# Performance work log

Hardware: AMD Instinct MI355X
Metric: run time of the kernel (lower is better)

The kernel has to match this reference:

```python
import jax, jax.numpy as jnp
import numpy as np

N_HEAD, D_K = 16, 64  # from init_kwargs (d_v == d_k)

def setup_inputs() -> dict:
    key = jax.random.key(0)
    ks = jax.random.split(key, 8)
    B, S, D, DFF = 8, 1024, 1024, 4096
    s = 1.0 / np.sqrt(D)
    return {
        "enc_input": jax.random.normal(ks[0], (B, S, D), jnp.float32),
        "mask": jnp.ones((B, 1, S), jnp.int32),
        "gap": 1,
        "wq": jax.random.normal(ks[1], (D, N_HEAD * D_K), jnp.float32) * s,
        "wk": jax.random.normal(ks[2], (D, N_HEAD * D_K), jnp.float32) * s,
        "wv": jax.random.normal(ks[3], (D, N_HEAD * D_K), jnp.float32) * s,
        "wo": jax.random.normal(ks[4], (N_HEAD * D_K, D), jnp.float32) * s,
        "w1": jax.random.normal(ks[5], (D, DFF), jnp.float32) * s,
        "b1": jnp.zeros((DFF,), jnp.float32),
        "w2": jax.random.normal(ks[6], (DFF, D), jnp.float32) * (1.0 / np.sqrt(DFF)),
        "b2": jnp.zeros((D,), jnp.float32),
    }

def reference(enc_input, mask, gap, wq, wk, wv, wo, w1, b1, w2, b2):
    # dropout=0, use_layer_norm=0, adapter=0 are hard-coded in EncoderLayer.__init__
    B, S, D = enc_input.shape
    H, dk = N_HEAD, D_K
    temperature = dk ** 0.5

    q = (enc_input @ wq).reshape(B, S, H, dk).transpose(0, 2, 1, 3)  # [B,H,S,dk]
    k = (enc_input @ wk).reshape(B, S, H, dk).transpose(0, 2, 1, 3)
    v = (enc_input @ wv).reshape(B, S, H, dk).transpose(0, 2, 1, 3)

    attn = jnp.einsum('bhqd,bhkd->bhqk', q / temperature, k)  # [B,H,S,S]
    # mask [B,1,S] -> unsqueeze head dim -> [B,1,1,S]
    attn = jnp.where(mask[:, None] == 0, jnp.float32(-1e9), attn)
    attn = jax.nn.softmax(attn, axis=-1)

    ctx = jnp.einsum('bhqk,bhkd->bhqd', attn, v)          # [B,H,S,dk]
    ctx = ctx.transpose(0, 2, 1, 3).reshape(B, S, H * dk)  # [B,S,D]
    enc = ctx @ wo + enc_input                              # attn residual

    ffn = jax.nn.relu(enc @ w1 + b1) @ w2 + b2
    out = ffn + enc                                         # ffn residual
    return out, attn
```

## Files before the change

kernel.cpp:

```cpp
#include <hip/hip_runtime.h>
#include <hip/hip_bf16.h>
#include <stdint.h>

typedef __bf16 bf16x8 __attribute__((ext_vector_type(8)));
typedef float  f32x4  __attribute__((ext_vector_type(4)));

typedef __attribute__((address_space(1))) void gvoid;
typedef __attribute__((address_space(3))) void lvoid;

__device__ __forceinline__ void async16(void* lds, const void* g) {
    __builtin_amdgcn_global_load_lds((gvoid*)g, (lvoid*)lds, 16, 0, 0);
}

__device__ __forceinline__ float fexp2(float x) {
    return __builtin_amdgcn_exp2f(x);
}

__global__ void prep_all(const float* __restrict__ X, __hip_bfloat16* __restrict__ Xb,
                         const float* __restrict__ wq, const float* __restrict__ wk,
                         const float* __restrict__ wv, const float* __restrict__ wo,
                         const float* __restrict__ w1, const float* __restrict__ w2,
                         __hip_bfloat16* __restrict__ Wcat,
                         __hip_bfloat16* __restrict__ Wot,
                         __hip_bfloat16* __restrict__ W1t,
                         __hip_bfloat16* __restrict__ W2t) {
    const int tix = blockIdx.x;
    if (tix >= 12288) {
        const int bi = tix - 12288;
        const int tid = threadIdx.y * 32 + threadIdx.x;
        const long i = ((long)bi * 256 + tid) * 4;
        float4 v = *(const float4*)(X + i);
        __hip_bfloat162* d = (__hip_bfloat162*)(Xb + i);
        d[0] = __float22bfloat162_rn(make_float2(v.x, v.y));
        d[1] = __float22bfloat162_rn(make_float2(v.z, v.w));
        return;
    }
    __shared__ float t[32][33];
    const float* in;
    __hip_bfloat16* out;
    int R, C, cx, cy;
    if (tix < 4096) {
        int wid = tix >> 10, tile = tix & 1023;
        const float* srcs[4] = {wq, wk, wv, wo};
        __hip_bfloat16* dsts[4] = {Wcat, Wcat + 1024 * 1024, Wcat + 2 * 1024 * 1024, Wot};
        in = srcs[wid]; out = dsts[wid];
        R = 1024; C = 1024; cx = tile & 31; cy = tile >> 5;
    } else if (tix < 8192) {
        int tile = tix - 4096;
        in = w1; out = W1t; R = 1024; C = 4096;
        cx = tile & 127; cy = tile >> 7;
    } else {
        int tile = tix - 8192;
        in = w2; out = W2t; R = 4096; C = 1024;
        cx = tile & 31; cy = tile >> 5;
    }
    const int c0 = cx * 32, r0 = cy * 32;
    const int tx = threadIdx.x, ty = threadIdx.y;
#pragma unroll
    for (int i = 0; i < 4; ++i) {
        int r = r0 + ty + i * 8;
        t[ty + i * 8][tx] = in[(long)r * C + c0 + tx];
    }
    __syncthreads();
#pragma unroll
    for (int i = 0; i < 4; ++i) {
        int c = c0 + ty + i * 8;
        out[(long)c * R + r0 + tx] = __float2bfloat16(t[tx][ty + i * 8]);
    }
}

#define RBAR asm volatile("s_barrier" ::: "memory")

__global__ void __launch_bounds__(256, 2)
attn_fused(const __hip_bfloat16* __restrict__ QKb,
           const __hip_bfloat16* __restrict__ Vt,
           const int* __restrict__ mask,
           float* __restrict__ attn,
           __hip_bfloat16* __restrict__ Ctx) {
    __shared__ __align__(16) __hip_bfloat16 sK[128 * 64];
    __shared__ __align__(16) __hip_bfloat16 sV[2][64 * 128];
    __shared__ __align__(16) __hip_bfloat16 sP[128 * 64];
    __shared__ float smadd[1024];

    const int tid = threadIdx.x, lane = tid & 63, wave = tid >> 6;
    const int r16 = lane & 15, kg = lane >> 4;
    const float SC2 = 0.125f * 1.44269504f;

    const int dd = blockIdx.x;
    const int wgt = (dd & 7) * 128 + (dd >> 3);
    const int xblk = wgt & 7, z = wgt >> 3;
    const int b = z >> 4, h = z & 15;
    const int row0 = xblk * 128;
    const int wrow = wave * 32;

    const __hip_bfloat16* Qz = QKb + ((long)b * 1024 + row0) * 2048 + h * 64;
    const __hip_bfloat16* Kz = QKb + (long)b * 1024 * 2048 + 1024 + h * 64;
    const __hip_bfloat16* Vz = Vt + (long)z * 64 * 1024;
    float* attnZ = attn + (long)z * 1024 * 1024 + (long)row0 * 1024;

    for (int i = tid; i < 1024; i += 256)
        smadd[i] = mask[b * 1024 + i] ? 0.f : -1.5e9f;

    bf16x8 qa[2][2];
#pragma unroll
    for (int m = 0; m < 2; ++m)
#pragma unroll
        for (int kf = 0; kf < 2; ++kf)
            qa[m][kf] = *(const bf16x8*)(Qz + (long)(wrow + m * 16 + r16) * 2048 + kf * 32 + kg * 8);

    float lrow[2][4];
#pragma unroll
    for (int m = 0; m < 2; ++m)
#pragma unroll
        for (int i = 0; i < 4; ++i) lrow[m][i] = 0.f;

    const int ssw = (r16 & 7) << 4;

    auto stageK = [&](char* dst, int ct) {
#pragma unroll
        for (int j = 0; j < 4; ++j) {
            int c = wave * 4 + j;
            int s = c * 8 + (lane >> 3);
            int cb = (lane & 7) * 16;
            async16(dst + c * 1024,
                    (const char*)(Kz + (long)(ct * 128 + s) * 2048) + (cb ^ ((s & 7) << 4)));
        }
    };
    auto stageV = [&](int ct, int buf) {
#pragma unroll
        for (int j = 0; j < 4; ++j) {
            int c = wave * 4 + j;
            int dv = c * 4 + (lane >> 4);
            int cb = (lane & 15) * 16;
            async16((char*)sV[buf] + c * 1024,
                    (const char*)(Vz + (long)dv * 1024 + ct * 128) + (cb ^ ((dv & 7) << 4)));
        }
    };

    char* kbuf0 = (char*)sK;
    char* kbuf1 = (char*)sP;
    stageK(kbuf0, 0);

    for (int ct = 0; ct < 8; ++ct) {
        asm volatile("s_waitcnt vmcnt(0)" ::: "memory");
        __syncthreads();
        if (ct < 7) stageK((ct & 1) ? kbuf0 : kbuf1, ct + 1);
        const char* base = (ct & 1) ? kbuf1 : kbuf0;

        f32x4 sacc[2][8];
#pragma unroll
        for (int m = 0; m < 2; ++m)
#pragma unroll
            for (int nf = 0; nf < 8; ++nf) sacc[m][nf] = f32x4{0.f, 0.f, 0.f, 0.f};

        __builtin_amdgcn_s_setprio(1);
#pragma unroll
        for (int nf = 0; nf < 8; ++nf) {
            const char* kr = base + (nf * 16 + r16) * 128;
            bf16x8 bv0 = *(const bf16x8*)(kr + ((kg * 16) ^ ssw));
            bf16x8 bv1 = *(const bf16x8*)(kr + ((64 + kg * 16) ^ ssw));
#pragma unroll
            for (int m = 0; m < 2; ++m) {
                sacc[m][nf] = __builtin_amdgcn_mfma_f32_16x16x32_bf16(qa[m][0], bv0, sacc[m][nf], 0, 0, 0);
                sacc[m][nf] = __builtin_amdgcn_mfma_f32_16x16x32_bf16(qa[m][1], bv1, sacc[m][nf], 0, 0, 0);
            }
        }
        __builtin_amdgcn_s_setprio(0);

        float madd[8];
#pragma unroll
        for (int nf = 0; nf < 8; ++nf) madd[nf] = smadd[ct * 128 + nf * 16 + r16];

#pragma unroll
        for (int m = 0; m < 2; ++m)
#pragma unroll
            for (int i = 0; i < 4; ++i) {
                float ts = 0.f;
#pragma unroll
                for (int nf = 0; nf < 8; ++nf)
                    ts += fexp2(sacc[m][nf][i] * SC2 + madd[nf]);
#pragma unroll
                for (int o = 1; o < 16; o <<= 1) ts += __shfl_xor(ts, o);
                lrow[m][i] += ts;
            }
    }

    float rinv[2][4];
#pragma unroll
    for (int m = 0; m < 2; ++m)
#pragma unroll
        for (int i = 0; i < 4; ++i) rinv[m][i] = 1.0f / lrow[m][i];

    f32x4 oacc[2][4];
#pragma unroll
    for (int m = 0; m < 2; ++m)
#pragma unroll
        for (int nf = 0; nf < 4; ++nf) oacc[m][nf] = f32x4{0.f, 0.f, 0.f, 0.f};

    __syncthreads();
    stageK((char*)sK, 0);
    stageV(0, 0);
    asm volatile("s_waitcnt vmcnt(0)" ::: "memory");
    __syncthreads();

    for (int ct = 0; ct < 8; ++ct) {
        f32x4 sacc[2][8];
#pragma unroll
        for (int m = 0; m < 2; ++m)
#pragma unroll
            for (int nf = 0; nf < 8; ++nf) sacc[m][nf] = f32x4{0.f, 0.f, 0.f, 0.f};

        __builtin_amdgcn_s_setprio(1);
#pragma unroll
        for (int nf = 0; nf < 8; ++nf) {
            const char* kr = (const char*)sK + (nf * 16 + r16) * 128;
            bf16x8 bv0 = *(const bf16x8*)(kr + ((kg * 16) ^ ssw));
            bf16x8 bv1 = *(const bf16x8*)(kr + ((64 + kg * 16) ^ ssw));
#pragma unroll
            for (int m = 0; m < 2; ++m) {
                sacc[m][nf] = __builtin_amdgcn_mfma_f32_16x16x32_bf16(qa[m][0], bv0, sacc[m][nf], 0, 0, 0);
                sacc[m][nf] = __builtin_amdgcn_mfma_f32_16x16x32_bf16(qa[m][1], bv1, sacc[m][nf], 0, 0, 0);
            }
        }
        __builtin_amdgcn_s_setprio(0);

        RBAR;
        if (ct < 7) {
            stageK((char*)sK, ct + 1);
            stageV(ct + 1, (ct + 1) & 1);
        }
        asm volatile("" ::: "memory");

        float madd[8];
#pragma unroll
        for (int nf = 0; nf < 8; ++nf) madd[nf] = smadd[ct * 128 + nf * 16 + r16];

        const char* sVb = (const char*)sV[ct & 1];

#pragma unroll
        for (int half = 0; half < 2; ++half) {
#pragma unroll
            for (int m = 0; m < 2; ++m)
#pragma unroll
                for (int nf = 0; nf < 4; ++nf) {
                    const int nfg = half * 4 + nf;
                    const int scol = nfg * 16 + r16;
                    const int scl = nf * 16 + r16;
#pragma unroll
                    for (int i = 0; i < 4; ++i) {
                        int q = wrow + m * 16 + kg * 4 + i;
                        float p = fexp2(sacc[m][nfg][i] * SC2 + madd[nfg]) * rinv[m][i];
                        __builtin_nontemporal_store(p, attnZ + (long)q * 1024 + ct * 128 + scol);
                        *(__hip_bfloat16*)((char*)sP + q * 128 + ((scl * 2) ^ ((q & 7) << 4))) =
                            __float2bfloat16(p);
                    }
                }

            __builtin_amdgcn_s_setprio(1);
#pragma unroll
            for (int ks = 0; ks < 2; ++ks) {
                const int ksg = half * 2 + ks;
                bf16x8 pa[2], vv[4];
#pragma unroll
                for (int m = 0; m < 2; ++m)
                    pa[m] = *(const bf16x8*)((const char*)sP + (wrow + m * 16 + r16) * 128 +
                                             ((ks * 64 + kg * 16) ^ ssw));
#pragma unroll
                for (int nf = 0; nf < 4; ++nf)
                    vv[nf] = *(const bf16x8*)(sVb + (nf * 16 + r16) * 256 +
                                              ((ksg * 64 + kg * 16) ^ ssw));
#pragma unroll
                for (int m = 0; m < 2; ++m)
#pragma unroll
                    for (int nf = 0; nf < 4; ++nf)
                        oacc[m][nf] = __builtin_amdgcn_mfma_f32_16x16x32_bf16(pa[m], vv[nf], oacc[m][nf], 0, 0, 0);
            }
            __builtin_amdgcn_s_setprio(0);
        }

        if (ct < 7) {
            asm volatile("s_waitcnt vmcnt(63)" ::: "memory");
            RBAR;
        }
    }

#pragma unroll
    for (int m = 0; m < 2; ++m)
#pragma unroll
        for (int nf = 0; nf < 4; ++nf)
#pragma unroll
            for (int i = 0; i < 4; ++i) {
                int q = wrow + m * 16 + kg * 4 + i;
                Ctx[((long)b * 1024 + row0 + q) * 1024 + h * 64 + nf * 16 + r16] =
                    __float2bfloat16(oacc[m][nf][i]);
            }
}

#define RDA(BUF, PM, ML, KS) \
    (*(const bf16x8*)(aRd + (BUF)*32768 + (PM)*16384 + (ML)*2048 + ((((KS)*64) + kg*16) ^ sw)))
#define RDB(BUF, PN, NL, KS) \
    (*(const bf16x8*)(bRd + (BUF)*32768 + (PN)*16384 + (NL)*2048 + ((((KS)*64) + kg*16) ^ sw)))
#define LOAD_A(BUF, PM)                          \
    _Pragma("unroll") for (int ml = 0; ml < 4; ++ml) \
    _Pragma("unroll") for (int ks = 0; ks < 2; ++ks) \
        a[ml][ks] = RDA(BUF, PM, ml, ks)
#define LOAD_B(DST, BUF, PN)                     \
    _Pragma("unroll") for (int nl = 0; nl < 2; ++nl) \
    _Pragma("unroll") for (int ks = 0; ks < 2; ++ks) \
        DST[nl][ks] = RDB(BUF, PN, nl, ks)
#define MFMA16(PM, PN, BB)                                                   \
    __builtin_amdgcn_s_setprio(1);                                           \
    _Pragma("unroll") for (int ks = 0; ks < 2; ++ks)                         \
    _Pragma("unroll") for (int ml = 0; ml < 4; ++ml)                         \
    _Pragma("unroll") for (int nl = 0; nl < 2; ++nl)                         \
        acc[(PM)*4 + ml][(PN)*2 + nl] = __builtin_amdgcn_mfma_f32_16x16x32_bf16( \
            a[ml][ks], BB[nl][ks], acc[(PM)*4 + ml][(PN)*2 + nl], 0, 0, 0);  \
    __builtin_amdgcn_s_setprio(0)
#define BAR asm volatile("s_barrier" ::: "memory")

__global__ void __launch_bounds__(512, 2)
gemm256(const __hip_bfloat16* __restrict__ A, int lda,
        const __hip_bfloat16* __restrict__ Bt, int ldb,
        int K, int Mtiles,
        const float* __restrict__ bias, int relu,
        __hip_bfloat16* __restrict__ C, int ldc) {
    __shared__ __align__(16) char lds[131072];
    const int NT = K >> 6;
    const int tid = threadIdx.x, lane = tid & 63, wave = tid >> 6;
    const int r16 = lane & 15, kg = lane >> 4;
    const int wr = wave >> 2, wc = wave & 3;
    const int sw = (r16 & 7) << 4;

    const int nwg = gridDim.x;
    const int q8 = nwg >> 3, r8 = nwg & 7;
    const int xcd = blockIdx.x & 7, rest = blockIdx.x >> 3;
    const int wg = (xcd < r8 ? xcd * (q8 + 1) : r8 * (q8 + 1) + (xcd - r8) * q8) + rest;
    const int tm = wg % Mtiles, tn = wg / Mtiles;
    const long row0 = (long)tm * 256, col0 = (long)tn * 256;

    const int idx = tid >> 3;
    const int slotp = ((tid & 7) ^ (idx & 7)) * 8;
    const __hip_bfloat16* aSrc[4];
    const __hip_bfloat16* bSrc[4];
#pragma unroll
    for (int j = 0; j < 4; ++j) {
        long ar = row0 + (j & 1) * 128 + (j >> 1) * 64 + idx;
        aSrc[j] = A + ar * lda + slotp;
        long br = col0 + ((j & 1) * 2 + (tid >> 8)) * 64 + (j >> 1) * 32 + (idx & 31);
        bSrc[j] = Bt + br * ldb + slotp;
    }

    char* ldsA = lds;
    char* ldsB = lds + 65536;
    const int stDst = wave * 1024;
    auto stA = [&](int v, int j) {
        async16(ldsA + ((v & 1) << 15) + (j << 13) + stDst, aSrc[j] + (v << 6));
    };
    auto stB = [&](int v, int j) {
        async16(ldsB + ((v & 1) << 15) + (j << 13) + stDst, bSrc[j] + (v << 6));
    };

    stA(0, 0); stA(0, 1); stB(0, 0); stB(0, 1);
    stA(0, 2); stA(0, 3); stB(0, 2); stB(0, 3);
    stA(1, 0); stA(1, 1); stB(1, 0); stB(1, 1);
    asm volatile("s_waitcnt vmcnt(4)" ::: "memory");
    BAR;

    f32x4 acc[8][4] = {};
    const char* aRd = ldsA + wr * 8192 + r16 * 128;
    const char* bRd = ldsB + wc * 4096 + r16 * 128;

    for (int u = 0; u < NT; u += 2) {
        const bool more = (u + 2) < NT;
        bf16x8 a[4][2], b0[2][2], b1[2][2];

        LOAD_A(0, 0);
        LOAD_B(b0, 0, 0);
        stA(u + 1, 2); stA(u + 1, 3);
        MFMA16(0, 0, b0);
        BAR;

        LOAD_B(b1, 0, 1);
        stB(u + 1, 2); stB(u + 1, 3);
        MFMA16(0, 1, b1);
        BAR;

        LOAD_A(0, 1);
        if (more) { stA(u + 2, 0); stA(u + 2, 1); }
        MFMA16(1, 0, b0);
        BAR;

        if (more) {
            stB(u + 2, 0); stB(u + 2, 1);
            asm volatile("s_waitcnt vmcnt(4)" ::: "memory");
        } else {
            asm volatile("s_waitcnt vmcnt(0)" ::: "memory");
        }
        MFMA16(1, 1, b1);
        BAR;

        LOAD_A(1, 0);
        LOAD_B(b0, 1, 0);
        if (more) { stA(u + 2, 2); stA(u + 2, 3); }
        MFMA16(0, 0, b0);
        BAR;

        LOAD_B(b1, 1, 1);
        if (more) { stB(u + 2, 2); stB(u + 2, 3); }
        MFMA16(0, 1, b1);
        BAR;

        LOAD_A(1, 1);
        if (more) { stA(u + 3, 0); stA(u + 3, 1); }
        MFMA16(1, 0, b0);
        BAR;

        if (more) {
            stB(u + 3, 0); stB(u + 3, 1);
            asm volatile("s_waitcnt vmcnt(4)" ::: "memory");
        }
        MFMA16(1, 1, b1);
        BAR;
    }

    const long crow = row0 + wr * 128, ccol = col0 + wc * 64;
#pragma unroll
    for (int mf = 0; mf < 8; ++mf)
#pragma unroll
        for (int nf = 0; nf < 4; ++nf) {
            const long col = ccol + nf * 16 + r16;
            const float bs = bias ? bias[col] : 0.f;
#pragma unroll
            for (int i = 0; i < 4; ++i) {
                const long row = crow + mf * 16 + kg * 4 + i;
                float v = acc[mf][nf][i] + bs;
                if (relu) v = fmaxf(v, 0.f);
                C[row * (long)ldc + col] = __float2bfloat16(v);
            }
        }
}

#define RDB128(BUF, NL, KS) \
    (*(const bf16x8*)(bRd + (BUF)*16384 + (NL)*2048 + ((((KS)*64) + kg*16) ^ sw)))
#define LOAD_B128(DST, BUF)                      \
    _Pragma("unroll") for (int nl = 0; nl < 2; ++nl) \
    _Pragma("unroll") for (int ks = 0; ks < 2; ++ks) \
        DST[nl][ks] = RDB128(BUF, nl, ks)
#define MFMA16N(PM, BB)                                                      \
    __builtin_amdgcn_s_setprio(1);                                           \
    _Pragma("unroll") for (int ks = 0; ks < 2; ++ks)                         \
    _Pragma("unroll") for (int ml = 0; ml < 4; ++ml)                         \
    _Pragma("unroll") for (int nl = 0; nl < 2; ++nl)                         \
        acc[(PM)*4 + ml][nl] = __builtin_amdgcn_mfma_f32_16x16x32_bf16(      \
            a[ml][ks], BB[nl][ks], acc[(PM)*4 + ml][nl], 0, 0, 0);           \
    __builtin_amdgcn_s_setprio(0)

__global__ void __launch_bounds__(512, 2)
gemm256n128(const __hip_bfloat16* __restrict__ A, int lda,
            const __hip_bfloat16* __restrict__ Bt, int ldb,
            int K, int Mtiles,
            const float* __restrict__ bias, int relu,
            const float* __restrict__ resf,
            const __hip_bfloat16* __restrict__ resb, int ldres,
            float* __restrict__ Cf, __hip_bfloat16* __restrict__ Cb, int ldc) {
    __shared__ __align__(16) char lds[98304];
    const int NT = K >> 6;
    const int tid = threadIdx.x, lane = tid & 63, wave = tid >> 6;
    const int r16 = lane & 15, kg = lane >> 4;
    const int wr = wave >> 2, wc = wave & 3;
    const int sw = (r16 & 7) << 4;

    const int nwg = gridDim.x;
    const int q8 = nwg >> 3, r8 = nwg & 7;
    const int xcd = blockIdx.x & 7, rest = blockIdx.x >> 3;
    const int wg = (xcd < r8 ? xcd * (q8 + 1) : r8 * (q8 + 1) + (xcd - r8) * q8) + rest;
    const int tm = wg % Mtiles, tn = wg / Mtiles;
    const long row0 = (long)tm * 256, col0 = (long)tn * 128;

    const int idx = tid >> 3;
    const int slotp = ((tid & 7) ^ (idx & 7)) * 8;
    const __hip_bfloat16* aSrc[4];
    const __hip_bfloat16* bSrc[2];
#pragma unroll
    for (int j = 0; j < 4; ++j) {
        long ar = row0 + (j & 1) * 128 + (j >> 1) * 64 + idx;
        aSrc[j] = A + ar * lda + slotp;
    }
#pragma unroll
    for (int j = 0; j < 2; ++j) {
        long br = col0 + j * 64 + idx;
        bSrc[j] = Bt + br * ldb + slotp;
    }

    char* ldsA = lds;
    char* ldsB = lds + 65536;
    const int stDst = wave * 1024;
    auto stA = [&](int v, int j) {
        async16(ldsA + ((v & 1) << 15) + (j << 13) + stDst, aSrc[j] + (v << 6));
    };
    auto stB = [&](int v, int j) {
        async16(ldsB + ((v & 1) << 14) + (j << 13) + stDst, bSrc[j] + (v << 6));
    };

    stA(0, 0); stA(0, 1); stA(0, 2); stA(0, 3);
    stB(0, 0); stB(0, 1);
    stA(1, 0); stA(1, 1);
    stB(1, 0); stB(1, 1);
    asm volatile("s_waitcnt vmcnt(4)" ::: "memory");
    BAR;

    f32x4 acc[8][2] = {};
    const char* aRd = ldsA + wr * 8192 + r16 * 128;
    const char* bRd = ldsB + wc * 4096 + r16 * 128;

    for (int u = 0; u < NT; u += 2) {
        const bool more = (u + 2) < NT;
        bf16x8 a[4][2], b0[2][2], b1[2][2];

        LOAD_A(0, 0);
        LOAD_B128(b0, 0);
        stA(u + 1, 2); stA(u + 1, 3);
        MFMA16N(0, b0);
        BAR;

        LOAD_A(0, 1);
        if (more) {
            stA(u + 2, 0); stA(u + 2, 1);
            stB(u + 2, 0); stB(u + 2, 1);
            asm volatile("s_waitcnt vmcnt(4)" ::: "memory");
        } else {
            asm volatile("s_waitcnt vmcnt(0)" ::: "memory");
        }
        MFMA16N(1, b0);
        BAR;

        LOAD_A(1, 0);
        LOAD_B128(b1, 1);
        if (more) { stA(u + 2, 2); stA(u + 2, 3); }
        MFMA16N(0, b1);
        BAR;

        LOAD_A(1, 1);
        if (more) {
            stA(u + 3, 0); stA(u + 3, 1);
            stB(u + 3, 0); stB(u + 3, 1);
            asm volatile("s_waitcnt vmcnt(4)" ::: "memory");
        }
        MFMA16N(1, b1);
        BAR;
    }

    const long crow = row0 + wr * 128, ccol = col0 + wc * 32;
#pragma unroll
    for (int mf = 0; mf < 8; ++mf)
#pragma unroll
        for (int nf = 0; nf < 2; ++nf) {
            const long col = ccol + nf * 16 + r16;
            const float bs = bias ? bias[col] : 0.f;
#pragma unroll
            for (int i = 0; i < 4; ++i) {
                const long row = crow + mf * 16 + kg * 4 + i;
                float v = acc[mf][nf][i] + bs;
                if (relu) v = fmaxf(v, 0.f);
                if (resf) v += resf[row * (long)ldres + col];
                if (resb) v += __bfloat162float(resb[row * (long)ldres + col]);
                const long off = row * (long)ldc + col;
                if (Cf) Cf[off] = v;
                if (Cb) Cb[off] = __float2bfloat16(v);
            }
        }
}

__global__ void __launch_bounds__(512, 2)
gemm_v(const __hip_bfloat16* __restrict__ A, int lda,
       const __hip_bfloat16* __restrict__ Bt, int ldb,
       int K,
       __hip_bfloat16* __restrict__ Vt) {
    __shared__ __align__(16) char lds[98304];
    const int NT = K >> 6;
    const int tid = threadIdx.x, lane = tid & 63, wave = tid >> 6;
    const int r16 = lane & 15, kg = lane >> 4;
    const int wr = wave >> 2, wc = wave & 3;
    const int sw = (r16 & 7) << 4;

    const int nwg = gridDim.x;
    const int q8 = nwg >> 3, r8 = nwg & 7;
    const int xcd = blockIdx.x & 7, rest = blockIdx.x >> 3;
    const int wg = (xcd < r8 ? xcd * (q8 + 1) : r8 * (q8 + 1) + (xcd - r8) * q8) + rest;
    const int tm = wg & 31, tn = wg >> 5;
    const long row0 = (long)tm * 256, col0 = (long)tn * 128;

    const int idx = tid >> 3;
    const int slotp = ((tid & 7) ^ (idx & 7)) * 8;
    const __hip_bfloat16* aSrc[4];
    const __hip_bfloat16* bSrc[2];
#pragma unroll
    for (int j = 0; j < 4; ++j) {
        long ar = row0 + (j & 1) * 128 + (j >> 1) * 64 + idx;
        aSrc[j] = A + ar * lda + slotp;
    }
#pragma unroll
    for (int j = 0; j < 2; ++j) {
        long br = col0 + j * 64 + idx;
        bSrc[j] = Bt + br * ldb + slotp;
    }

    char* ldsA = lds;
    char* ldsB = lds + 65536;
    const int stDst = wave * 1024;
    auto stA = [&](int v, int j) {
        async16(ldsA + ((v & 1) << 15) + (j << 13) + stDst, aSrc[j] + (v << 6));
    };
    auto stB = [&](int v, int j) {
        async16(ldsB + ((v & 1) << 14) + (j << 13) + stDst, bSrc[j] + (v << 6));
    };

    stA(0, 0); stA(0, 1); stA(0, 2); stA(0, 3);
    stB(0, 0); stB(0, 1);
    stA(1, 0); stA(1, 1);
    stB(1, 0); stB(1, 1);
    asm volatile("s_waitcnt vmcnt(4)" ::: "memory");
    BAR;

    f32x4 acc[8][2] = {};
    const char* aRd = ldsA + wr * 8192 + r16 * 128;
    const char* bRd = ldsB + wc * 4096 + r16 * 128;

    for (int u = 0; u < NT; u += 2) {
        const bool more = (u + 2) < NT;
        bf16x8 a[4][2], b0[2][2], b1[2][2];

        LOAD_A(0, 0);
        LOAD_B128(b0, 0);
        stA(u + 1, 2); stA(u + 1, 3);
        MFMA16N(0, b0);
        BAR;

        LOAD_A(0, 1);
        if (more) {
            stA(u + 2, 0); stA(u + 2, 1);
            stB(u + 2, 0); stB(u + 2, 1);
            asm volatile("s_waitcnt vmcnt(4)" ::: "memory");
        } else {
            asm volatile("s_waitcnt vmcnt(0)" ::: "memory");
        }
        MFMA16N(1, b0);
        BAR;

        LOAD_A(1, 0);
        LOAD_B128(b1, 1);
        if (more) { stA(u + 2, 2); stA(u + 2, 3); }
        MFMA16N(0, b1);
        BAR;

        LOAD_A(1, 1);
        if (more) {
            stA(u + 3, 0); stA(u + 3, 1);
            stB(u + 3, 0); stB(u + 3, 1);
            asm volatile("s_waitcnt vmcnt(4)" ::: "memory");
        }
        MFMA16N(1, b1);
        BAR;
    }

    __hip_bfloat16* sT = (__hip_bfloat16*)lds;
    {
        const int cls = wc * 32;
        const int rls = wr * 128 + kg * 4;
#pragma unroll
        for (int mf = 0; mf < 8; ++mf)
#pragma unroll
            for (int nf = 0; nf < 2; ++nf) {
                int cl = cls + nf * 16 + r16;
                int rl = rls + mf * 16;
                __hip_bfloat162 lo = __float22bfloat162_rn(make_float2(acc[mf][nf][0], acc[mf][nf][1]));
                __hip_bfloat162 hi = __float22bfloat162_rn(make_float2(acc[mf][nf][2], acc[mf][nf][3]));
                *(__hip_bfloat162*)(&sT[cl * 264 + rl]) = lo;
                *(__hip_bfloat162*)(&sT[cl * 264 + rl + 2]) = hi;
            }
    }
    __syncthreads();
    {
        const int b = (int)(row0 >> 10);
        const int s_base = (int)(row0 & 1023);
#pragma unroll
        for (int j = 0; j < 8; ++j) {
            int dl = wave * 16 + j * 2 + (lane >> 5);
            int sc = (lane & 31) * 8;
            bf16x8 v = *(const bf16x8*)(&sT[dl * 264 + sc]);
            int dg = (int)col0 + dl;
            int z = b * 16 + (dg >> 6);
            int d = dg & 63;
            *(bf16x8*)(Vt + ((long)z * 64 + d) * 1024 + s_base + sc) = v;
        }
    }
}

extern "C" void kernel_launch(void* const* d_in, const int* in_sizes, int n_in,
                              void* d_out, int out_size, void* d_ws, size_t ws_size,
                              hipStream_t stream) {
    const int B = 8, S = 1024, D = 1024, DFF = 4096;
    const long SD = (long)B * S * D;

    const float* X  = (const float*)d_in[0];
    const int*  msk = (const int*)d_in[1];
    const float* wq = (const float*)d_in[3];
    const float* wk = (const float*)d_in[4];
    const float* wv = (const float*)d_in[5];
    const float* wo = (const float*)d_in[6];
    const float* w1 = (const float*)d_in[7];
    const float* b1 = (const float*)d_in[8];
    const float* w2 = (const float*)d_in[9];
    const float* b2 = (const float*)d_in[10];

    float* out  = (float*)d_out;
    float* attn = out + SD;

    char* ws = (char*)d_ws;
    auto alloc = [&](size_t bytes) {
        char* p = ws;
        ws += (bytes + 255) & ~(size_t)255;
        return p;
    };
    __hip_bfloat16* Xb   = (__hip_bfloat16*)alloc(SD * 2);
    __hip_bfloat16* QKb  = (__hip_bfloat16*)alloc(SD * 4);
    __hip_bfloat16* Vt   = (__hip_bfloat16*)alloc(SD * 2);
    __hip_bfloat16* Ctx  = (__hip_bfloat16*)alloc(SD * 2);
    __hip_bfloat16* EncB = (__hip_bfloat16*)alloc(SD * 2);
    __hip_bfloat16* Hb   = (__hip_bfloat16*)alloc((long)B * S * DFF * 2);
    __hip_bfloat16* Wcat = (__hip_bfloat16*)alloc((long)3 * D * D * 2);
    __hip_bfloat16* Wot  = (__hip_bfloat16*)alloc((long)D * D * 2);
    __hip_bfloat16* W1t  = (__hip_bfloat16*)alloc((long)D * DFF * 2);
    __hip_bfloat16* W2t  = (__hip_bfloat16*)alloc((long)D * DFF * 2);
    (void)ws_size; (void)in_sizes; (void)n_in; (void)out_size;

    dim3 tb(32, 8);
    prep_all<<<dim3(12288 + 8192), tb, 0, stream>>>(X, Xb, wq, wk, wv, wo, w1, w2,
                                                    Wcat, Wot, W1t, W2t);

    gemm256<<<dim3(32 * 8), 512, 0, stream>>>(
        Xb, D, Wcat, D, D, 32, nullptr, 0, QKb, 2048);

    gemm_v<<<dim3(32 * 8), 512, 0, stream>>>(
        Xb, D, Wcat + (long)2048 * 1024, D, D, Vt);

    attn_fused<<<dim3(1024), 256, 0, stream>>>(QKb, Vt, msk, attn, Ctx);

    gemm256n128<<<dim3(32 * 8), 512, 0, stream>>>(
        Ctx, D, Wot, D, D, 32,
        nullptr, 0, X, nullptr, D,
        nullptr, EncB, D);

    gemm256<<<dim3(32 * 16), 512, 0, stream>>>(
        EncB, D, W1t, D, D, 32, b1, 1, Hb, DFF);

    gemm256n128<<<dim3(32 * 8), 512, 0, stream>>>(
        Hb, DFF, W2t, DFF, DFF, 32,
        b2, 0, nullptr, EncB, D,
        out, nullptr, D);
}
```

Baseline: 500.8 us.

## Merge QK and V projection GEMMs into one launch; nontemporal fp32 stores

```diff
diff --git a/kernel.cpp b/kernel.cpp
--- a/kernel.cpp
+++ b/kernel.cpp
@@ -139,6 +139,7 @@
 
     char* kbuf0 = (char*)sK;
     char* kbuf1 = (char*)sP;
+    kbuf1 = (char*)sV[0];
     stageK(kbuf0, 0);
 
     for (int ct = 0; ct < 8; ++ct) {
@@ -317,129 +318,6 @@
             a[ml][ks], BB[nl][ks], acc[(PM)*4 + ml][(PN)*2 + nl], 0, 0, 0);  \
     __builtin_amdgcn_s_setprio(0)
 #define BAR asm volatile("s_barrier" ::: "memory")
-
-__global__ void __launch_bounds__(512, 2)
-gemm256(const __hip_bfloat16* __restrict__ A, int lda,
-        const __hip_bfloat16* __restrict__ Bt, int ldb,
-        int K, int Mtiles,
-        const float* __restrict__ bias, int relu,
-        __hip_bfloat16* __restrict__ C, int ldc) {
-    __shared__ __align__(16) char lds[131072];
-    const int NT = K >> 6;
-    const int tid = threadIdx.x, lane = tid & 63, wave = tid >> 6;
-    const int r16 = lane & 15, kg = lane >> 4;
-    const int wr = wave >> 2, wc = wave & 3;
-    const int sw = (r16 & 7) << 4;
-
-    const int nwg = gridDim.x;
-    const int q8 = nwg >> 3, r8 = nwg & 7;
-    const int xcd = blockIdx.x & 7, rest = blockIdx.x >> 3;
-    const int wg = (xcd < r8 ? xcd * (q8 + 1) : r8 * (q8 + 1) + (xcd - r8) * q8) + rest;
-    const int tm = wg % Mtiles, tn = wg / Mtiles;
-    const long row0 = (long)tm * 256, col0 = (long)tn * 256;
-
-    const int idx = tid >> 3;
-    const int slotp = ((tid & 7) ^ (idx & 7)) * 8;
-    const __hip_bfloat16* aSrc[4];
-    const __hip_bfloat16* bSrc[4];
-#pragma unroll
-    for (int j = 0; j < 4; ++j) {
-        long ar = row0 + (j & 1) * 128 + (j >> 1) * 64 + idx;
-        aSrc[j] = A + ar * lda + slotp;
-        long br = col0 + ((j & 1) * 2 + (tid >> 8)) * 64 + (j >> 1) * 32 + (idx & 31);
-        bSrc[j] = Bt + br * ldb + slotp;
-    }
-
-    char* ldsA = lds;
-    char* ldsB = lds + 65536;
-    const int stDst = wave * 1024;
-    auto stA = [&](int v, int j) {
-        async16(ldsA + ((v & 1) << 15) + (j << 13) + stDst, aSrc[j] + (v << 6));
-    };
-    auto stB = [&](int v, int j) {
-        async16(ldsB + ((v & 1) << 15) + (j << 13) + stDst, bSrc[j] + (v << 6));
-    };
-
-    stA(0, 0); stA(0, 1); stB(0, 0); stB(0, 1);
-    stA(0, 2); stA(0, 3); stB(0, 2); stB(0, 3);
-    stA(1, 0); stA(1, 1); stB(1, 0); stB(1, 1);
-    asm volatile("s_waitcnt vmcnt(4)" ::: "memory");
-    BAR;
-
-    f32x4 acc[8][4] = {};
-    const char* aRd = ldsA + wr * 8192 + r16 * 128;
-    const char* bRd = ldsB + wc * 4096 + r16 * 128;
-
-    for (int u = 0; u < NT; u += 2) {
-        const bool more = (u + 2) < NT;
-        bf16x8 a[4][2], b0[2][2], b1[2][2];
-
-        LOAD_A(0, 0);
-        LOAD_B(b0, 0, 0);
-        stA(u + 1, 2); stA(u + 1, 3);
-        MFMA16(0, 0, b0);
-        BAR;
-
-        LOAD_B(b1, 0, 1);
-        stB(u + 1, 2); stB(u + 1, 3);
-        MFMA16(0, 1, b1);
-        BAR;
-
-        LOAD_A(0, 1);
-        if (more) { stA(u + 2, 0); stA(u + 2, 1); }
-        MFMA16(1, 0, b0);
-        BAR;
-
-        if (more) {
-            stB(u + 2, 0); stB(u + 2, 1);
-            asm volatile("s_waitcnt vmcnt(4)" ::: "memory");
-        } else {
-            asm volatile("s_waitcnt vmcnt(0)" ::: "memory");
-        }
-        MFMA16(1, 1, b1);
-        BAR;
-
-        LOAD_A(1, 0);
-        LOAD_B(b0, 1, 0);
-        if (more) { stA(u + 2, 2); stA(u + 2, 3); }
-        MFMA16(0, 0, b0);
-        BAR;
-
-        LOAD_B(b1, 1, 1);
-        if (more) { stB(u + 2, 2); stB(u + 2, 3); }
-        MFMA16(0, 1, b1);
-        BAR;
-
-        LOAD_A(1, 1);
-        if (more) { stA(u + 3, 0); stA(u + 3, 1); }
-        MFMA16(1, 0, b0);
-        BAR;
-
-        if (more) {
-            stB(u + 3, 0); stB(u + 3, 1);
-            asm volatile("s_waitcnt vmcnt(4)" ::: "memory");
-        }
-        MFMA16(1, 1, b1);
-        BAR;
-    }
-
-    const long crow = row0 + wr * 128, ccol = col0 + wc * 64;
-#pragma unroll
-    for (int mf = 0; mf < 8; ++mf)
-#pragma unroll
-        for (int nf = 0; nf < 4; ++nf) {
-            const long col = ccol + nf * 16 + r16;
-            const float bs = bias ? bias[col] : 0.f;
-#pragma unroll
-            for (int i = 0; i < 4; ++i) {
-                const long row = crow + mf * 16 + kg * 4 + i;
-                float v = acc[mf][nf][i] + bs;
-                if (relu) v = fmaxf(v, 0.f);
-                C[row * (long)ldc + col] = __float2bfloat16(v);
-            }
-        }
-}
-
 #define RDB128(BUF, NL, KS) \
     (*(const bf16x8*)(bRd + (BUF)*16384 + (NL)*2048 + ((((KS)*64) + kg*16) ^ sw)))
 #define LOAD_B128(DST, BUF)                      \
@@ -456,6 +334,356 @@
     __builtin_amdgcn_s_setprio(0)
 
 __global__ void __launch_bounds__(512, 2)
+gemm256(const __hip_bfloat16* __restrict__ A, int lda,
+        const __hip_bfloat16* __restrict__ Bt, int ldb,
+        int K, int Mtiles,
+        const float* __restrict__ bias, int relu,
+        __hip_bfloat16* __restrict__ C, int ldc) {
+    __shared__ __align__(16) char lds[131072];
+    const int NT = K >> 6;
+    const int tid = threadIdx.x, lane = tid & 63, wave = tid >> 6;
+    const int r16 = lane & 15, kg = lane >> 4;
+    const int wr = wave >> 2, wc = wave & 3;
+    const int sw = (r16 & 7) << 4;
+
+    const int nwg = gridDim.x;
+    const int q8 = nwg >> 3, r8 = nwg & 7;
+    const int xcd = blockIdx.x & 7, rest = blockIdx.x >> 3;
+    const int wg = (xcd < r8 ? xcd * (q8 + 1) : r8 * (q8 + 1) + (xcd - r8) * q8) + rest;
+    const int tm = wg % Mtiles, tn = wg / Mtiles;
+    const long row0 = (long)tm * 256, col0 = (long)tn * 256;
+
+    const int idx = tid >> 3;
+    const int slotp = ((tid & 7) ^ (idx & 7)) * 8;
+    const __hip_bfloat16* aSrc[4];
+    const __hip_bfloat16* bSrc[4];
+#pragma unroll
+    for (int j = 0; j < 4; ++j) {
+        long ar = row0 + (j & 1) * 128 + (j >> 1) * 64 + idx;
+        aSrc[j] = A + ar * lda + slotp;
+        long br = col0 + ((j & 1) * 2 + (tid >> 8)) * 64 + (j >> 1) * 32 + (idx & 31);
+        bSrc[j] = Bt + br * ldb + slotp;
+    }
+
+    char* ldsA = lds;
+    char* ldsB = lds + 65536;
+    const int stDst = wave * 1024;
+    auto stA = [&](int v, int j) {
+        async16(ldsA + ((v & 1) << 15) + (j << 13) + stDst, aSrc[j] + (v << 6));
+    };
+    auto stB = [&](int v, int j) {
+        async16(ldsB + ((v & 1) << 15) + (j << 13) + stDst, bSrc[j] + (v << 6));
+    };
+
+    stA(0, 0); stA(0, 1); stB(0, 0); stB(0, 1);
+    stA(0, 2); stA(0, 3); stB(0, 2); stB(0, 3);
+    stA(1, 0); stA(1, 1); stB(1, 0); stB(1, 1);
+    asm volatile("s_waitcnt vmcnt(4)" ::: "memory");
+    BAR;
+
+    f32x4 acc[8][4] = {};
+    const char* aRd = ldsA + wr * 8192 + r16 * 128;
+    const char* bRd = ldsB + wc * 4096 + r16 * 128;
+
+    for (int u = 0; u < NT; u += 2) {
+        const bool more = (u + 2) < NT;
+        bf16x8 a[4][2], b0[2][2], b1[2][2];
+
+        LOAD_A(0, 0);
+        LOAD_B(b0, 0, 0);
+        stA(u + 1, 2); stA(u + 1, 3);
+        MFMA16(0, 0, b0);
+        BAR;
+
+        LOAD_B(b1, 0, 1);
+        stB(u + 1, 2); stB(u + 1, 3);
+        MFMA16(0, 1, b1);
+        BAR;
+
+        LOAD_A(0, 1);
+        if (more) { stA(u + 2, 0); stA(u + 2, 1); }
+        MFMA16(1, 0, b0);
+        BAR;
+
+        if (more) {
+            stB(u + 2, 0); stB(u + 2, 1);
+            asm volatile("s_waitcnt vmcnt(4)" ::: "memory");
+        } else {
+            asm volatile("s_waitcnt vmcnt(0)" ::: "memory");
+        }
+        MFMA16(1, 1, b1);
+        BAR;
+
+        LOAD_A(1, 0);
+        LOAD_B(b0, 1, 0);
+        if (more) { stA(u + 2, 2); stA(u + 2, 3); }
+        MFMA16(0, 0, b0);
+        BAR;
+
+        LOAD_B(b1, 1, 1);
+        if (more) { stB(u + 2, 2); stB(u + 2, 3); }
+        MFMA16(0, 1, b1);
+        BAR;
+
+        LOAD_A(1, 1);
+        if (more) { stA(u + 3, 0); stA(u + 3, 1); }
+        MFMA16(1, 0, b0);
+        BAR;
+
+        if (more) {
+            stB(u + 3, 0); stB(u + 3, 1);
+            asm volatile("s_waitcnt vmcnt(4)" ::: "memory");
+        }
+        MFMA16(1, 1, b1);
+        BAR;
+    }
+
+    const long crow = row0 + wr * 128, ccol = col0 + wc * 64;
+#pragma unroll
+    for (int mf = 0; mf < 8; ++mf)
+#pragma unroll
+        for (int nf = 0; nf < 4; ++nf) {
+            const long col = ccol + nf * 16 + r16;
+            const float bs = bias ? bias[col] : 0.f;
+#pragma unroll
+            for (int i = 0; i < 4; ++i) {
+                const long row = crow + mf * 16 + kg * 4 + i;
+                float v = acc[mf][nf][i] + bs;
+                if (relu) v = fmaxf(v, 0.f);
+                C[row * (long)ldc + col] = __float2bfloat16(v);
+            }
+        }
+}
+
+__global__ void __launch_bounds__(512, 2)
+gemm_qkv(const __hip_bfloat16* __restrict__ A,
+         const __hip_bfloat16* __restrict__ Wcat,
+         __hip_bfloat16* __restrict__ QKb,
+         __hip_bfloat16* __restrict__ Vt) {
+    __shared__ __align__(16) char lds[131072];
+    const int tid = threadIdx.x, lane = tid & 63, wave = tid >> 6;
+    const int r16 = lane & 15, kg = lane >> 4;
+    const int wr = wave >> 2, wc = wave & 3;
+    const int sw = (r16 & 7) << 4;
+    const int idx = tid >> 3;
+    const int slotp = ((tid & 7) ^ (idx & 7)) * 8;
+    const int stDst = wave * 1024;
+    constexpr int NT = 16;
+
+    if (blockIdx.x < 256) {
+        const int id = blockIdx.x;
+        const int xcd = id & 7, rest = id >> 3;
+        const int wg = xcd * 32 + rest;
+        const int tm = wg & 31, tn = wg >> 5;
+        const long row0 = (long)tm * 256, col0 = (long)tn * 256;
+
+        const __hip_bfloat16* aSrc[4];
+        const __hip_bfloat16* bSrc[4];
+#pragma unroll
+        for (int j = 0; j < 4; ++j) {
+            long ar = row0 + (j & 1) * 128 + (j >> 1) * 64 + idx;
+            aSrc[j] = A + ar * 1024 + slotp;
+            long br = col0 + ((j & 1) * 2 + (tid >> 8)) * 64 + (j >> 1) * 32 + (idx & 31);
+            bSrc[j] = Wcat + br * 1024 + slotp;
+        }
+
+        char* ldsA = lds;
+        char* ldsB = lds + 65536;
+        auto stA = [&](int v, int j) {
+            async16(ldsA + ((v & 1) << 15) + (j << 13) + stDst, aSrc[j] + (v << 6));
+        };
+        auto stB = [&](int v, int j) {
+            async16(ldsB + ((v & 1) << 15) + (j << 13) + stDst, bSrc[j] + (v << 6));
+        };
+
+        stA(0, 0); stA(0, 1); stB(0, 0); stB(0, 1);
+        stA(0, 2); stA(0, 3); stB(0, 2); stB(0, 3);
+        stA(1, 0); stA(1, 1); stB(1, 0); stB(1, 1);
+        asm volatile("s_waitcnt vmcnt(4)" ::: "memory");
+        BAR;
+
+        f32x4 acc[8][4] = {};
+        const char* aRd = ldsA + wr * 8192 + r16 * 128;
+        const char* bRd = ldsB + wc * 4096 + r16 * 128;
+
+        for (int u = 0; u < NT; u += 2) {
+            const bool more = (u + 2) < NT;
+            bf16x8 a[4][2], b0[2][2], b1[2][2];
+
+            LOAD_A(0, 0);
+            LOAD_B(b0, 0, 0);
+            stA(u + 1, 2); stA(u + 1, 3);
+            MFMA16(0, 0, b0);
+            BAR;
+
+            LOAD_B(b1, 0, 1);
+            stB(u + 1, 2); stB(u + 1, 3);
+            MFMA16(0, 1, b1);
+            BAR;
+
+            LOAD_A(0, 1);
+            if (more) { stA(u + 2, 0); stA(u + 2, 1); }
+            MFMA16(1, 0, b0);
+            BAR;
+
+            if (more) {
+                stB(u + 2, 0); stB(u + 2, 1);
+                asm volatile("s_waitcnt vmcnt(4)" ::: "memory");
+            } else {
+                asm volatile("s_waitcnt vmcnt(0)" ::: "memory");
+            }
+            MFMA16(1, 1, b1);
+            BAR;
+
+            LOAD_A(1, 0);
+            LOAD_B(b0, 1, 0);
+            if (more) { stA(u + 2, 2); stA(u + 2, 3); }
+            MFMA16(0, 0, b0);
+            BAR;
+
+            LOAD_B(b1, 1, 1);
+            if (more) { stB(u + 2, 2); stB(u + 2, 3); }
+            MFMA16(0, 1, b1);
+            BAR;
+
+            LOAD_A(1, 1);
+            if (more) { stA(u + 3, 0); stA(u + 3, 1); }
+            MFMA16(1, 0, b0);
+            BAR;
+
+            if (more) {
+                stB(u + 3, 0); stB(u + 3, 1);
+                asm volatile("s_waitcnt vmcnt(4)" ::: "memory");
+            }
+            MFMA16(1, 1, b1);
+            BAR;
+        }
+
+        const long crow = row0 + wr * 128, ccol = col0 + wc * 64;
+#pragma unroll
+        for (int mf = 0; mf < 8; ++mf)
+#pragma unroll
+            for (int nf = 0; nf < 4; ++nf) {
+                const long col = ccol + nf * 16 + r16;
+#pragma unroll
+                for (int i = 0; i < 4; ++i) {
+                    const long row = crow + mf * 16 + kg * 4 + i;
+                    QKb[row * 2048 + col] = __float2bfloat16(acc[mf][nf][i]);
+                }
+            }
+    } else {
+        const int id = blockIdx.x - 256;
+        const int xcd = id & 7, rest = id >> 3;
+        const int wg = xcd * 32 + rest;
+        const int tm = wg & 31, tn = wg >> 5;
+        const long row0 = (long)tm * 256, col0 = (long)tn * 128;
+        const __hip_bfloat16* Bt = Wcat + (long)2048 * 1024;
+
+        const __hip_bfloat16* aSrc[4];
+        const __hip_bfloat16* bSrc[2];
+#pragma unroll
+        for (int j = 0; j < 4; ++j) {
+            long ar = row0 + (j & 1) * 128 + (j >> 1) * 64 + idx;
+            aSrc[j] = A + ar * 1024 + slotp;
+        }
+#pragma unroll
+        for (int j = 0; j < 2; ++j) {
+            long br = col0 + j * 64 + idx;
+            bSrc[j] = Bt + br * 1024 + slotp;
+        }
+
+        char* ldsA = lds;
+        char* ldsB = lds + 65536;
+        auto stA = [&](int v, int j) {
+            async16(ldsA + ((v & 1) << 15) + (j << 13) + stDst, aSrc[j] + (v << 6));
+        };
+        auto stB = [&](int v, int j) {
+            async16(ldsB + ((v & 1) << 14) + (j << 13) + stDst, bSrc[j] + (v << 6));
+        };
+
+        stA(0, 0); stA(0, 1); stA(0, 2); stA(0, 3);
+        stB(0, 0); stB(0, 1);
+        stA(1, 0); stA(1, 1);
+        stB(1, 0); stB(1, 1);
+        asm volatile("s_waitcnt vmcnt(4)" ::: "memory");
+        BAR;
+
+        f32x4 acc[8][2] = {};
+        const char* aRd = ldsA + wr * 8192 + r16 * 128;
+        const char* bRd = ldsB + wc * 4096 + r16 * 128;
+
+        for (int u = 0; u < NT; u += 2) {
+            const bool more = (u + 2) < NT;
+            bf16x8 a[4][2], b0[2][2], b1[2][2];
+
+            LOAD_A(0, 0);
+            LOAD_B128(b0, 0);
+            stA(u + 1, 2); stA(u + 1, 3);
+            MFMA16N(0, b0);
+            BAR;
+
+            LOAD_A(0, 1);
+            if (more) {
+                stA(u + 2, 0); stA(u + 2, 1);
+                stB(u + 2, 0); stB(u + 2, 1);
+                asm volatile("s_waitcnt vmcnt(4)" ::: "memory");
+            } else {
+                asm volatile("s_waitcnt vmcnt(0)" ::: "memory");
+            }
+            MFMA16N(1, b0);
+            BAR;
+
+            LOAD_A(1, 0);
+            LOAD_B128(b1, 1);
+            if (more) { stA(u + 2, 2); stA(u + 2, 3); }
+            MFMA16N(0, b1);
+            BAR;
+
+            LOAD_A(1, 1);
+            if (more) {
+                stA(u + 3, 0); stA(u + 3, 1);
+                stB(u + 3, 0); stB(u + 3, 1);
+                asm volatile("s_waitcnt vmcnt(4)" ::: "memory");
+            }
+            MFMA16N(1, b1);
+            BAR;
+        }
+
+        __hip_bfloat16* sT = (__hip_bfloat16*)lds;
+        {
+            const int cls = wc * 32;
+            const int rls = wr * 128 + kg * 4;
+#pragma unroll
+            for (int mf = 0; mf < 8; ++mf)
+#pragma unroll
+                for (int nf = 0; nf < 2; ++nf) {
+                    int cl = cls + nf * 16 + r16;
+                    int rl = rls + mf * 16;
+                    __hip_bfloat162 lo = __float22bfloat162_rn(make_float2(acc[mf][nf][0], acc[mf][nf][1]));
+                    __hip_bfloat162 hi = __float22bfloat162_rn(make_float2(acc[mf][nf][2], acc[mf][nf][3]));
+                    *(__hip_bfloat162*)(&sT[cl * 264 + rl]) = lo;
+                    *(__hip_bfloat162*)(&sT[cl * 264 + rl + 2]) = hi;
+                }
+        }
+        __syncthreads();
+        {
+            const int b = (int)(row0 >> 10);
+            const int s_base = (int)(row0 & 1023);
+#pragma unroll
+            for (int j = 0; j < 8; ++j) {
+                int dl = wave * 16 + j * 2 + (lane >> 5);
+                int sc = (lane & 31) * 8;
+                bf16x8 v = *(const bf16x8*)(&sT[dl * 264 + sc]);
+                int dg = (int)col0 + dl;
+                int z = b * 16 + (dg >> 6);
+                int d = dg & 63;
+                *(bf16x8*)(Vt + ((long)z * 64 + d) * 1024 + s_base + sc) = v;
+            }
+        }
+    }
+}
+
+__global__ void __launch_bounds__(512, 2)
 gemm256n128(const __hip_bfloat16* __restrict__ A, int lda,
             const __hip_bfloat16* __restrict__ Bt, int ldb,
             int K, int Mtiles,
@@ -565,135 +793,10 @@
                 if (resf) v += resf[row * (long)ldres + col];
                 if (resb) v += __bfloat162float(resb[row * (long)ldres + col]);
                 const long off = row * (long)ldc + col;
-                if (Cf) Cf[off] = v;
+                if (Cf) __builtin_nontemporal_store(v, Cf + off);
                 if (Cb) Cb[off] = __float2bfloat16(v);
             }
         }
-}
-
-__global__ void __launch_bounds__(512, 2)
-gemm_v(const __hip_bfloat16* __restrict__ A, int lda,
-       const __hip_bfloat16* __restrict__ Bt, int ldb,
-       int K,
-       __hip_bfloat16* __restrict__ Vt) {
-    __shared__ __align__(16) char lds[98304];
-    const int NT = K >> 6;
-    const int tid = threadIdx.x, lane = tid & 63, wave = tid >> 6;
-    const int r16 = lane & 15, kg = lane >> 4;
-    const int wr = wave >> 2, wc = wave & 3;
-    const int sw = (r16 & 7) << 4;
-
-    const int nwg = gridDim.x;
-    const int q8 = nwg >> 3, r8 = nwg & 7;
-    const int xcd = blockIdx.x & 7, rest = blockIdx.x >> 3;
-    const int wg = (xcd < r8 ? xcd * (q8 + 1) : r8 * (q8 + 1) + (xcd - r8) * q8) + rest;
-    const int tm = wg & 31, tn = wg >> 5;
-    const long row0 = (long)tm * 256, col0 = (long)tn * 128;
-
-    const int idx = tid >> 3;
-    const int slotp = ((tid & 7) ^ (idx & 7)) * 8;
-    const __hip_bfloat16* aSrc[4];
-    const __hip_bfloat16* bSrc[2];
-#pragma unroll
-    for (int j = 0; j < 4; ++j) {
-        long ar = row0 + (j & 1) * 128 + (j >> 1) * 64 + idx;
-        aSrc[j] = A + ar * lda + slotp;
-    }
-#pragma unroll
-    for (int j = 0; j < 2; ++j) {
-        long br = col0 + j * 64 + idx;
-        bSrc[j] = Bt + br * ldb + slotp;
-    }
-
-    char* ldsA = lds;
-    char* ldsB = lds + 65536;
-    const int stDst = wave * 1024;
-    auto stA = [&](int v, int j) {
-        async16(ldsA + ((v & 1) << 15) + (j << 13) + stDst, aSrc[j] + (v << 6));
-    };
-    auto stB = [&](int v, int j) {
-        async16(ldsB + ((v & 1) << 14) + (j << 13) + stDst, bSrc[j] + (v << 6));
-    };
-
-    stA(0, 0); stA(0, 1); stA(0, 2); stA(0, 3);
-    stB(0, 0); stB(0, 1);
-    stA(1, 0); stA(1, 1);
-    stB(1, 0); stB(1, 1);
-    asm volatile("s_waitcnt vmcnt(4)" ::: "memory");
-    BAR;
-
-    f32x4 acc[8][2] = {};
-    const char* aRd = ldsA + wr * 8192 + r16 * 128;
-    const char* bRd = ldsB + wc * 4096 + r16 * 128;
-
-    for (int u = 0; u < NT; u += 2) {
-        const bool more = (u + 2) < NT;
-        bf16x8 a[4][2], b0[2][2], b1[2][2];
-
-        LOAD_A(0, 0);
-        LOAD_B128(b0, 0);
-        stA(u + 1, 2); stA(u + 1, 3);
-        MFMA16N(0, b0);
-        BAR;
-
-        LOAD_A(0, 1);
-        if (more) {
-            stA(u + 2, 0); stA(u + 2, 1);
-            stB(u + 2, 0); stB(u + 2, 1);
-            asm volatile("s_waitcnt vmcnt(4)" ::: "memory");
-        } else {
-            asm volatile("s_waitcnt vmcnt(0)" ::: "memory");
-        }
-        MFMA16N(1, b0);
-        BAR;
-
-        LOAD_A(1, 0);
-        LOAD_B128(b1, 1);
-        if (more) { stA(u + 2, 2); stA(u + 2, 3); }
-        MFMA16N(0, b1);
-        BAR;
-
-        LOAD_A(1, 1);
-        if (more) {
-            stA(u + 3, 0); stA(u + 3, 1);
-            stB(u + 3, 0); stB(u + 3, 1);
-            asm volatile("s_waitcnt vmcnt(4)" ::: "memory");
-        }
-        MFMA16N(1, b1);
-        BAR;
-    }
-
-    __hip_bfloat16* sT = (__hip_bfloat16*)lds;
-    {
-        const int cls = wc * 32;
-        const int rls = wr * 128 + kg * 4;
-#pragma unroll
-        for (int mf = 0; mf < 8; ++mf)
-#pragma unroll
-            for (int nf = 0; nf < 2; ++nf) {
-                int cl = cls + nf * 16 + r16;
-                int rl = rls + mf * 16;
-                __hip_bfloat162 lo = __float22bfloat162_rn(make_float2(acc[mf][nf][0], acc[mf][nf][1]));
-                __hip_bfloat162 hi = __float22bfloat162_rn(make_float2(acc[mf][nf][2], acc[mf][nf][3]));
-                *(__hip_bfloat162*)(&sT[cl * 264 + rl]) = lo;
-                *(__hip_bfloat162*)(&sT[cl * 264 + rl + 2]) = hi;
-            }
-    }
-    __syncthreads();
-    {
-        const int b = (int)(row0 >> 10);
-        const int s_base = (int)(row0 & 1023);
-#pragma unroll
-        for (int j = 0; j < 8; ++j) {
-            int dl = wave * 16 + j * 2 + (lane >> 5);
-            int sc = (lane & 31) * 8;
-            bf16x8 v = *(const bf16x8*)(&sT[dl * 264 + sc]);
-            int dg = (int)col0 + dl;
-            int z = b * 16 + (dg >> 6);
-            int d = dg & 63;
-            *(bf16x8*)(Vt + ((long)z * 64 + d) * 1024 + s_base + sc) = v;
-        }
-    }
 }
 
 extern "C" void kernel_launch(void* const* d_in, const int* in_sizes, int n_in,
@@ -738,11 +841,7 @@
     prep_all<<<dim3(12288 + 8192), tb, 0, stream>>>(X, Xb, wq, wk, wv, wo, w1, w2,
                                                     Wcat, Wot, W1t, W2t);
 
-    gemm256<<<dim3(32 * 8), 512, 0, stream>>>(
-        Xb, D, Wcat, D, D, 32, nullptr, 0, QKb, 2048);
-
-    gemm_v<<<dim3(32 * 8), 512, 0, stream>>>(
-        Xb, D, Wcat + (long)2048 * 1024, D, D, Vt);
+    gemm_qkv<<<dim3(512), 512, 0, stream>>>(Xb, Wcat, QKb, Vt);
 
     attn_fused<<<dim3(1024), 256, 0, stream>>>(QKb, Vt, msk, attn, Ctx);
 
```

After: 492.7 us. About the same (-1.6%).
